# Optimization experiments

Hardware: AMD Instinct MI355X
Metric: run time of the kernel (lower is better)

## Reference

```python
import jax, jax.numpy as jnp
import numpy as np

B, S, D_IN, D_H = 16, 4096, 512, 512

def setup_inputs() -> dict:
    key = jax.random.key(0)
    ks = jax.random.split(key, 8)
    inp = {
        "input": jax.random.normal(ks[0], (B, D_IN), dtype=jnp.float32),
        "context": jax.random.normal(ks[1], (B, S, D_IN), dtype=jnp.float32),
        "mask": jax.random.bernoulli(ks[2], 0.2, (B, S)),
        # parameters (torch nn.Linear layout: W [out,in], b [out])
        "W_in": jax.random.normal(ks[3], (D_H, D_IN), dtype=jnp.float32) / np.sqrt(D_IN),
        "b_in": jax.random.normal(ks[4], (D_H,), dtype=jnp.float32) * 0.01,
        "W_ctx": jax.random.normal(ks[5], (D_H, D_IN), dtype=jnp.float32) / np.sqrt(D_IN),
        "b_ctx": jax.random.normal(ks[6], (D_H,), dtype=jnp.float32) * 0.01,
        "v": jax.random.normal(ks[7], (D_H,), dtype=jnp.float32),
    }
    return inp


def reference(input, context, mask, W_in, b_in, W_ctx, b_ctx, v):
    # inp: [B, H] projected decoder state
    inp = input @ W_in.T + b_in
    # ctx: [B, S, H] projected context (this is what the torch code matmuls
    # with the softmax weights, i.e. hidden lives in hidden_dim space)
    ctx = context @ W_ctx.T + b_ctx
    # additive (Bahdanau) scores: v . tanh(inp + ctx) -> [B, S]
    scores = jnp.einsum("h,bsh->bs", v, jnp.tanh(inp[:, None, :] + ctx))
    # masked positions get -inf so they receive zero softmax weight
    scores = jnp.where(mask, -jnp.inf, scores)
    attn = jax.nn.softmax(scores, axis=-1)  # [B, S]
    # weighted sum of projected context: [B, H]
    hidden = jnp.einsum("bsh,bs->bh", ctx, attn)
    return hidden, attn
```

## Files before the change

### kernel.cpp

```cpp
#include <hip/hip_runtime.h>
#include <hip/hip_bf16.h>

#define B_  16
#define S_  4096
#define DIN 512
#define DH  512

typedef _Float16 f16x8 __attribute__((ext_vector_type(8)));
typedef _Float16 f16x4 __attribute__((ext_vector_type(4)));
typedef float    f32x4 __attribute__((ext_vector_type(4)));


__device__ __forceinline__ float fast_tanh(float x) {
    float e = __expf(2.f * x);
    return 1.f - 2.f * __builtin_amdgcn_rcpf(e + 1.f);
}

__device__ __forceinline__ void gload_lds16(const void* g, void* l) {
    __builtin_amdgcn_global_load_lds(
        (const __attribute__((address_space(1))) void*)g,
        (__attribute__((address_space(3))) void*)l, 16, 0, 0);
}

__device__ __forceinline__ int mask_at(const void* mask, int isByte, int idx) {
    return isByte ? (int)((const unsigned char*)mask)[idx]
                  : ((const int*)mask)[idx];
}

__global__ void prep_kernel(const float* __restrict__ input,
                            const float* __restrict__ W_in,
                            const float* __restrict__ b_in,
                            const float* __restrict__ W_ctx,
                            const float* __restrict__ b_ctx,
                            const void*  __restrict__ mask,
                            _Float16* __restrict__ W16,
                            float* __restrict__ addv,
                            float* __restrict__ zeroRegion,
                            int* __restrict__ maskflag) {
    int blk = blockIdx.x;
    int tid = threadIdx.x;
    if (blk < 256) {
        int base = blk * 1024 + tid * 4;
        float4 wv = *(const float4*)(W_ctx + base);
        union { _Float16 f[4]; ushort4 u; } cv;
        cv.f[0] = (_Float16)wv.x; cv.f[1] = (_Float16)wv.y;
        cv.f[2] = (_Float16)wv.z; cv.f[3] = (_Float16)wv.w;
        *(ushort4*)(W16 + base) = cv.u;
    } else if (blk < 288) {
        int t = blk - 256;
        int b = t >> 1;
        int h = ((t & 1) << 8) + tid;
        __shared__ float inrow[DIN];
        inrow[tid]       = input[b * DIN + tid];
        inrow[tid + 256] = input[b * DIN + tid + 256];
        __syncthreads();
        const float* wr = W_in + (size_t)h * DIN;
        float acc = 0.f;
        for (int k = 0; k < DIN; k += 4) {
            float4 w4 = *(const float4*)(wr + k);
            acc += w4.x * inrow[k] + w4.y * inrow[k + 1]
                 + w4.z * inrow[k + 2] + w4.w * inrow[k + 3];
        }
        addv[b * DH + h] = acc + b_in[h] + b_ctx[h];
    } else if (blk == 288) {
        const uint4* m4 = (const uint4*)mask;
        unsigned int orw = 0;
#pragma unroll
        for (int it = 0; it < 16; ++it) {
            uint4 w = m4[it * 256 + tid];
            orw |= (w.x | w.y | w.z | w.w);
        }
        int found = ((orw & 0xFFFFFF00u) != 0) ? 1 : 0;
        __shared__ int f;
        if (tid == 0) f = 0;
        __syncthreads();
        if (found) atomicOr(&f, 1);
        __syncthreads();
        if (tid == 0) maskflag[0] = f;
    } else {
        int base = (blk - 289) * 4096;
#pragma unroll
        for (int it = 0; it < 16; ++it)
            zeroRegion[base + it * 256 + tid] = 0.f;
    }
}

__global__ __launch_bounds__(256)
void score_kernel(const float* __restrict__ context,
                  const _Float16* __restrict__ W16,
                  const float* __restrict__ addv,
                  const float* __restrict__ v,
                  float* __restrict__ scores) {
    __shared__ __align__(16) _Float16 As[2][4096];
    __shared__ __align__(16) _Float16 Bs[2][4096];

    const int tid  = threadIdx.x;
    const int wave = tid >> 6;
    const int lane = tid & 63;
    const int l15  = lane & 15;
    const int q    = lane >> 4;
    const int sg   = wave >> 1;
    const int ng   = wave & 1;

    const int xcd  = blockIdx.x & 7;
    const int slot = blockIdx.x >> 3;
    const int nt   = slot & 3;
    const int g    = (slot >> 2) * 8 + xcd;
    const int b    = g >> 5;
    const int st   = g & 31;
    const int s0   = st * 128;
    const int n0   = nt * 128;

    const float* ctxA = context + ((size_t)b * S_ + s0) * DIN;

#define STAGE_B(kc_, buf_)                                                     \
    {                                                                          \
        _Pragma("unroll")                                                      \
        for (int u = 0; u < 2; ++u) {                                          \
            int jn = wave * 2 + u;                                             \
            const _Float16* gp = W16 +                                         \
                (size_t)(n0 + jn * 16 + l15) * DIN + (kc_) * 32 + q * 8;       \
            gload_lds16(gp, &Bs[buf_][jn * 512]);                              \
        }                                                                      \
    }

    float4 areg[4];
#define LOADA(kc_)                                                             \
    {                                                                          \
        _Pragma("unroll")                                                      \
        for (int u = 0; u < 4; ++u) {                                          \
            int sgi = u * 256 + tid;                                           \
            int row = sgi >> 3, p = sgi & 7;                                   \
            areg[u] = *(const float4*)(ctxA + (size_t)row * DIN +              \
                                       (kc_) * 32 + p * 4);                    \
        }                                                                      \
    }

#define WRITEA(buf_)                                                           \
    {                                                                          \
        _Pragma("unroll")                                                      \
        for (int u = 0; u < 4; ++u) {                                          \
            int sgi = u * 256 + tid;                                           \
            int row = sgi >> 3, p = sgi & 7;                                   \
            int off = (row >> 4) * 512 + (p >> 1) * 128 + (row & 15) * 8 +     \
                      (p & 1) * 4;                                             \
            f16x4 hv;                                                          \
            hv[0] = (_Float16)areg[u].x; hv[1] = (_Float16)areg[u].y;          \
            hv[2] = (_Float16)areg[u].z; hv[3] = (_Float16)areg[u].w;          \
            *(f16x4*)&As[buf_][off] = hv;                                      \
        }                                                                      \
    }

    f32x4 acc[4][4];
#pragma unroll
    for (int jm = 0; jm < 4; ++jm)
#pragma unroll
        for (int jn = 0; jn < 4; ++jn) acc[jm][jn] = (f32x4){0.f, 0.f, 0.f, 0.f};

    STAGE_B(0, 0);
    LOADA(0);
    WRITEA(0);
    __syncthreads();

    for (int kc = 0; kc < 16; ++kc) {
        const int cur = kc & 1, nxt = cur ^ 1;
        if (kc + 1 < 16) {
            STAGE_B(kc + 1, nxt);
            LOADA(kc + 1);
        }

        f16x8 afr[4], bfr[4];
#pragma unroll
        for (int jm = 0; jm < 4; ++jm)
            afr[jm] = *(const f16x8*)&As[cur][(sg * 4 + jm) * 512 + q * 128 + l15 * 8];
#pragma unroll
        for (int jn = 0; jn < 4; ++jn)
            bfr[jn] = *(const f16x8*)&Bs[cur][(ng * 4 + jn) * 512 + q * 128 + l15 * 8];

#pragma unroll
        for (int jn = 0; jn < 4; ++jn)
#pragma unroll
            for (int jm = 0; jm < 4; ++jm)
                acc[jm][jn] = __builtin_amdgcn_mfma_f32_16x16x32_f16(
                    afr[jm], bfr[jn], acc[jm][jn], 0, 0, 0);

        if (kc + 1 < 16) WRITEA(nxt);
        __syncthreads();
    }

    const float* avb = addv + b * DH;
    float rowsum[4][4] = {{0.f,0.f,0.f,0.f},{0.f,0.f,0.f,0.f},
                          {0.f,0.f,0.f,0.f},{0.f,0.f,0.f,0.f}};
#pragma unroll
    for (int jn = 0; jn < 4; ++jn) {
        int n = n0 + (ng * 4 + jn) * 16 + l15;
        float av = avb[n];
        float vv = v[n];
#pragma unroll
        for (int jm = 0; jm < 4; ++jm)
#pragma unroll
            for (int r = 0; r < 4; ++r)
                rowsum[jm][r] += vv * fast_tanh(acc[jm][jn][r] + av);
    }
#pragma unroll
    for (int jm = 0; jm < 4; ++jm)
#pragma unroll
        for (int r = 0; r < 4; ++r) {
            float s = rowsum[jm][r];
            s += __shfl_xor(s, 1, 16);
            s += __shfl_xor(s, 2, 16);
            s += __shfl_xor(s, 4, 16);
            s += __shfl_xor(s, 8, 16);
            if (l15 == 0) {
                int srow = s0 + (sg * 4 + jm) * 16 + q * 4 + r;
                atomicAdd(&scores[b * S_ + srow], s);
            }
        }
}

__global__ __launch_bounds__(1024)
void stats_kernel(const float* __restrict__ scores,
                  const void* __restrict__ mask,
                  const int* __restrict__ maskflag,
                  float* __restrict__ stats) {
    __shared__ float rbuf[32];
    int b = blockIdx.x, tid = threadIdx.x;
    int wv = tid >> 6, ln = tid & 63;
    int isByte = maskflag[0];
    const float* sr = scores + b * S_;

    float mx = -__builtin_inff();
    float vals[4];
#pragma unroll
    for (int it = 0; it < 4; ++it) {
        int s = it * 1024 + tid;
        float x = mask_at(mask, isByte, b * S_ + s) ? -__builtin_inff() : sr[s];
        vals[it] = x;
        mx = fmaxf(mx, x);
    }
    for (int o = 1; o < 64; o <<= 1) mx = fmaxf(mx, __shfl_xor(mx, o, 64));
    if (ln == 0) rbuf[wv] = mx;
    __syncthreads();
    float m2 = rbuf[0];
#pragma unroll
    for (int i = 1; i < 16; ++i) m2 = fmaxf(m2, rbuf[i]);
    mx = m2;

    float sum = 0.f;
#pragma unroll
    for (int it = 0; it < 4; ++it) sum += __expf(vals[it] - mx);
    for (int o = 1; o < 64; o <<= 1) sum += __shfl_xor(sum, o, 64);
    if (ln == 0) rbuf[16 + wv] = sum;
    __syncthreads();
    if (tid == 0) {
        float t = 0.f;
#pragma unroll
        for (int i = 0; i < 16; ++i) t += rbuf[16 + i];
        stats[b * 2]     = mx;
        stats[b * 2 + 1] = 1.f / t;
    }
}

__global__ __launch_bounds__(256)
void attnwsum_kernel(const float* __restrict__ scores,
                     const float* __restrict__ context,
                     const void* __restrict__ mask,
                     const int* __restrict__ maskflag,
                     const float* __restrict__ stats,
                     float* __restrict__ attn,
                     float* __restrict__ wsum) {
    __shared__ int   selIdx[64];
    __shared__ float selW[64];
    __shared__ int   selCount;

    int b  = blockIdx.x >> 6;
    int c0 = (blockIdx.x & 63) * 64;
    int tid = threadIdx.x;
    int isByte = maskflag[0];
    float mx  = stats[b * 2];
    float inv = stats[b * 2 + 1];

    if (tid == 0) selCount = 0;
    __syncthreads();

    if (tid < 64) {
        int s = c0 + tid;
        int idx = b * S_ + s;
        float sc = mask_at(mask, isByte, idx) ? -__builtin_inff() : scores[idx];
        float p = __expf(sc - mx) * inv;
        attn[idx] = p;
        if (p > 1e-9f) {
            int k = atomicAdd(&selCount, 1);
            selIdx[k] = s;
            selW[k]  = p;
        }
    }
    __syncthreads();

    int cnt = selCount;
    if (cnt == 0) return;
    const float* cb = context + (size_t)b * S_ * DIN;
    float a00 = 0.f, a01 = 0.f, a10 = 0.f, a11 = 0.f;
    float a20 = 0.f, a21 = 0.f, a30 = 0.f, a31 = 0.f;
    int i = 0;
    for (; i + 4 <= cnt; i += 4) {
        const float* c0p = cb + (size_t)selIdx[i]     * DIN;
        const float* c1p = cb + (size_t)selIdx[i + 1] * DIN;
        const float* c2p = cb + (size_t)selIdx[i + 2] * DIN;
        const float* c3p = cb + (size_t)selIdx[i + 3] * DIN;
        float w0 = selW[i], w1 = selW[i + 1], w2 = selW[i + 2], w3 = selW[i + 3];
        a00 += w0 * c0p[tid]; a01 += w0 * c0p[tid + 256];
        a10 += w1 * c1p[tid]; a11 += w1 * c1p[tid + 256];
        a20 += w2 * c2p[tid]; a21 += w2 * c2p[tid + 256];
        a30 += w3 * c3p[tid]; a31 += w3 * c3p[tid + 256];
    }
    float acc0 = (a00 + a10) + (a20 + a30);
    float acc1 = (a01 + a11) + (a21 + a31);
    for (; i < cnt; ++i) {
        const float* cr = cb + (size_t)selIdx[i] * DIN;
        float w = selW[i];
        acc0 += w * cr[tid];
        acc1 += w * cr[tid + 256];
    }
    atomicAdd(&wsum[b * DIN + tid], acc0);
    atomicAdd(&wsum[b * DIN + tid + 256], acc1);
}

__global__ __launch_bounds__(256)
void hidden_kernel(const float* __restrict__ W_ctx,
                   const float* __restrict__ b_ctx,
                   const float* __restrict__ wsum,
                   float* __restrict__ hidden) {
    int b = blockIdx.x >> 1;
    int tid = threadIdx.x;
    int h = ((blockIdx.x & 1) << 8) + tid;
    __shared__ float wrow[DIN];
    wrow[tid]       = wsum[b * DIN + tid];
    wrow[tid + 256] = wsum[b * DIN + tid + 256];
    __syncthreads();
    const float* wr = W_ctx + (size_t)h * DIN;
    float acc = 0.f;
    for (int k = 0; k < DIN; k += 4) {
        float4 w4 = *(const float4*)(wr + k);
        acc += w4.x * wrow[k] + w4.y * wrow[k + 1]
             + w4.z * wrow[k + 2] + w4.w * wrow[k + 3];
    }
    hidden[b * DH + h] = acc + b_ctx[h];
}

extern "C" void kernel_launch(void* const* d_in, const int* in_sizes, int n_in,
                              void* d_out, int out_size, void* d_ws, size_t ws_size,
                              hipStream_t stream) {
    const float* input   = (const float*)d_in[0];
    const float* context = (const float*)d_in[1];
    const void*  mask    = d_in[2];
    const float* W_in    = (const float*)d_in[3];
    const float* b_in    = (const float*)d_in[4];
    const float* W_ctx   = (const float*)d_in[5];
    const float* b_ctx   = (const float*)d_in[6];
    const float* v       = (const float*)d_in[7];

    char* ws = (char*)d_ws;
    _Float16* W16   = (_Float16*)ws;
    float* addv     = (float*)(ws + 524288);
    float* scores   = (float*)(ws + 557056);
    float* wsum     = (float*)(ws + 819200);
    int*   maskflag = (int*)(ws + 851968);
    float* stats    = (float*)(ws + 852096);

    float* hidden = (float*)d_out;
    float* attn   = (float*)d_out + B_ * DH;

    prep_kernel<<<355, 256, 0, stream>>>(input, W_in, b_in, W_ctx, b_ctx, mask,
                                         W16, addv, scores , maskflag);
    score_kernel<<<2048, 256, 0, stream>>>(context, W16, addv, v, scores);
    stats_kernel<<<B_, 1024, 0, stream>>>(scores, mask, maskflag, stats);
    attnwsum_kernel<<<B_ * 64, 256, 0, stream>>>(scores, context, mask, maskflag,
                                                 stats, attn, wsum);
    hidden_kernel<<<B_ * 2, 256, 0, stream>>>(W_ctx, b_ctx, wsum, hidden);
}
```

Measured before the change: 312.7 us.

## Precast context to fp16 and stage it via direct LDS loads; fuse softmax stats

Adds a pass in the prep kernel that converts the whole context tensor to fp16 in workspace. The score GEMM then streams both operands with global-to-LDS loads instead of register loads plus conversion and LDS writes, which simplifies the loop to one barrier per step. The separate softmax-statistics kernel is removed, and each attention block recomputes its row's max and sum redundantly. The tradeoff is an extra full read and half-size write of the large context tensor, plus a larger workspace.

```diff
diff --git a/kernel.cpp b/kernel.cpp
--- a/kernel.cpp
+++ b/kernel.cpp
@@ -7,7 +7,6 @@
 #define DH  512
 
 typedef _Float16 f16x8 __attribute__((ext_vector_type(8)));
-typedef _Float16 f16x4 __attribute__((ext_vector_type(4)));
 typedef float    f32x4 __attribute__((ext_vector_type(4)));
 
 
@@ -27,27 +26,40 @@
                   : ((const int*)mask)[idx];
 }
 
-__global__ void prep_kernel(const float* __restrict__ input,
-                            const float* __restrict__ W_in,
-                            const float* __restrict__ b_in,
-                            const float* __restrict__ W_ctx,
-                            const float* __restrict__ b_ctx,
-                            const void*  __restrict__ mask,
-                            _Float16* __restrict__ W16,
-                            float* __restrict__ addv,
-                            float* __restrict__ zeroRegion,
-                            int* __restrict__ maskflag) {
+__global__ __launch_bounds__(256)
+void prep_kernel(const float* __restrict__ input,
+                 const float* __restrict__ W_in,
+                 const float* __restrict__ b_in,
+                 const float* __restrict__ context,
+                 const float* __restrict__ W_ctx,
+                 const float* __restrict__ b_ctx,
+                 const void*  __restrict__ mask,
+                 _Float16* __restrict__ W16,
+                 _Float16* __restrict__ ctx16,
+                 float* __restrict__ addv,
+                 float* __restrict__ zeroRegion,
+                 int* __restrict__ maskflag) {
     int blk = blockIdx.x;
     int tid = threadIdx.x;
-    if (blk < 256) {
-        int base = blk * 1024 + tid * 4;
+    if (blk < 8192) {
+#pragma unroll
+        for (int it = 0; it < 4; ++it) {
+            int base = blk * 4096 + it * 1024 + tid * 4;
+            float4 wv = *(const float4*)(context + base);
+            union { _Float16 f[4]; ushort4 u; } cv;
+            cv.f[0] = (_Float16)wv.x; cv.f[1] = (_Float16)wv.y;
+            cv.f[2] = (_Float16)wv.z; cv.f[3] = (_Float16)wv.w;
+            *(ushort4*)(ctx16 + base) = cv.u;
+        }
+    } else if (blk < 8448) {
+        int base = (blk - 8192) * 1024 + tid * 4;
         float4 wv = *(const float4*)(W_ctx + base);
         union { _Float16 f[4]; ushort4 u; } cv;
         cv.f[0] = (_Float16)wv.x; cv.f[1] = (_Float16)wv.y;
         cv.f[2] = (_Float16)wv.z; cv.f[3] = (_Float16)wv.w;
         *(ushort4*)(W16 + base) = cv.u;
-    } else if (blk < 288) {
-        int t = blk - 256;
+    } else if (blk < 8480) {
+        int t = blk - 8448;
         int b = t >> 1;
         int h = ((t & 1) << 8) + tid;
         __shared__ float inrow[DIN];
@@ -62,7 +74,7 @@
                  + w4.z * inrow[k + 2] + w4.w * inrow[k + 3];
         }
         addv[b * DH + h] = acc + b_in[h] + b_ctx[h];
-    } else if (blk == 288) {
+    } else if (blk == 8480) {
         const uint4* m4 = (const uint4*)mask;
         unsigned int orw = 0;
 #pragma unroll
@@ -78,7 +90,7 @@
         __syncthreads();
         if (tid == 0) maskflag[0] = f;
     } else {
-        int base = (blk - 289) * 4096;
+        int base = (blk - 8481) * 4096;
 #pragma unroll
         for (int it = 0; it < 16; ++it)
             zeroRegion[base + it * 256 + tid] = 0.f;
@@ -86,7 +98,7 @@
 }
 
 __global__ __launch_bounds__(256)
-void score_kernel(const float* __restrict__ context,
+void score_kernel(const _Float16* __restrict__ ctx16,
                   const _Float16* __restrict__ W16,
                   const float* __restrict__ addv,
                   const float* __restrict__ v,
@@ -111,71 +123,46 @@
     const int s0   = st * 128;
     const int n0   = nt * 128;
 
-    const float* ctxA = context + ((size_t)b * S_ + s0) * DIN;
-
-#define STAGE_B(kc_, buf_)                                                     \
-    {                                                                          \
-        _Pragma("unroll")                                                      \
-        for (int u = 0; u < 2; ++u) {                                          \
-            int jn = wave * 2 + u;                                             \
-            const _Float16* gp = W16 +                                         \
-                (size_t)(n0 + jn * 16 + l15) * DIN + (kc_) * 32 + q * 8;       \
-            gload_lds16(gp, &Bs[buf_][jn * 512]);                              \
-        }                                                                      \
-    }
-
-    float4 areg[4];
-#define LOADA(kc_)                                                             \
+    const _Float16* ctxA = ctx16 + ((size_t)b * S_ + s0) * DIN;
+
+#define STAGE(kc_, buf_)                                                       \
     {                                                                          \
         _Pragma("unroll")                                                      \
         for (int u = 0; u < 4; ++u) {                                          \
-            int sgi = u * 256 + tid;                                           \
-            int row = sgi >> 3, p = sgi & 7;                                   \
-            areg[u] = *(const float4*)(ctxA + (size_t)row * DIN +              \
-                                       (kc_) * 32 + p * 4);                    \
+            int id = wave * 4 + u;                                             \
+            if (id < 8) {                                                      \
+                const _Float16* gp = ctxA +                                    \
+                    (size_t)(id * 16 + l15) * DIN + (kc_) * 32 + q * 8;        \
+                gload_lds16(gp, &As[buf_][id * 512]);                          \
+            } else {                                                           \
+                int jn = id - 8;                                               \
+                const _Float16* gp = W16 +                                     \
+                    (size_t)(n0 + jn * 16 + l15) * DIN + (kc_) * 32 + q * 8;   \
+                gload_lds16(gp, &Bs[buf_][jn * 512]);                          \
+            }                                                                  \
         }                                                                      \
     }
 
-#define WRITEA(buf_)                                                           \
-    {                                                                          \
-        _Pragma("unroll")                                                      \
-        for (int u = 0; u < 4; ++u) {                                          \
-            int sgi = u * 256 + tid;                                           \
-            int row = sgi >> 3, p = sgi & 7;                                   \
-            int off = (row >> 4) * 512 + (p >> 1) * 128 + (row & 15) * 8 +     \
-                      (p & 1) * 4;                                             \
-            f16x4 hv;                                                          \
-            hv[0] = (_Float16)areg[u].x; hv[1] = (_Float16)areg[u].y;          \
-            hv[2] = (_Float16)areg[u].z; hv[3] = (_Float16)areg[u].w;          \
-            *(f16x4*)&As[buf_][off] = hv;                                      \
-        }                                                                      \
-    }
-
     f32x4 acc[4][4];
 #pragma unroll
     for (int jm = 0; jm < 4; ++jm)
 #pragma unroll
         for (int jn = 0; jn < 4; ++jn) acc[jm][jn] = (f32x4){0.f, 0.f, 0.f, 0.f};
 
-    STAGE_B(0, 0);
-    LOADA(0);
-    WRITEA(0);
-    __syncthreads();
+    STAGE(0, 0);
 
     for (int kc = 0; kc < 16; ++kc) {
-        const int cur = kc & 1, nxt = cur ^ 1;
-        if (kc + 1 < 16) {
-            STAGE_B(kc + 1, nxt);
-            LOADA(kc + 1);
-        }
+        __syncthreads();
+        int buf = kc & 1;
+        if (kc + 1 < 16) STAGE(kc + 1, buf ^ 1);
 
         f16x8 afr[4], bfr[4];
 #pragma unroll
         for (int jm = 0; jm < 4; ++jm)
-            afr[jm] = *(const f16x8*)&As[cur][(sg * 4 + jm) * 512 + q * 128 + l15 * 8];
+            afr[jm] = *(const f16x8*)&As[buf][(sg * 4 + jm) * 512 + q * 128 + l15 * 8];
 #pragma unroll
         for (int jn = 0; jn < 4; ++jn)
-            bfr[jn] = *(const f16x8*)&Bs[cur][(ng * 4 + jn) * 512 + q * 128 + l15 * 8];
+            bfr[jn] = *(const f16x8*)&Bs[buf][(ng * 4 + jn) * 512 + q * 128 + l15 * 8];
 
 #pragma unroll
         for (int jn = 0; jn < 4; ++jn)
@@ -183,9 +170,6 @@
             for (int jm = 0; jm < 4; ++jm)
                 acc[jm][jn] = __builtin_amdgcn_mfma_f32_16x16x32_f16(
                     afr[jm], bfr[jn], acc[jm][jn], 0, 0, 0);
-
-        if (kc + 1 < 16) WRITEA(nxt);
-        __syncthreads();
     }
 
     const float* avb = addv + b * DH;
@@ -218,57 +202,14 @@
         }
 }
 
-__global__ __launch_bounds__(1024)
-void stats_kernel(const float* __restrict__ scores,
-                  const void* __restrict__ mask,
-                  const int* __restrict__ maskflag,
-                  float* __restrict__ stats) {
-    __shared__ float rbuf[32];
-    int b = blockIdx.x, tid = threadIdx.x;
-    int wv = tid >> 6, ln = tid & 63;
-    int isByte = maskflag[0];
-    const float* sr = scores + b * S_;
-
-    float mx = -__builtin_inff();
-    float vals[4];
-#pragma unroll
-    for (int it = 0; it < 4; ++it) {
-        int s = it * 1024 + tid;
-        float x = mask_at(mask, isByte, b * S_ + s) ? -__builtin_inff() : sr[s];
-        vals[it] = x;
-        mx = fmaxf(mx, x);
-    }
-    for (int o = 1; o < 64; o <<= 1) mx = fmaxf(mx, __shfl_xor(mx, o, 64));
-    if (ln == 0) rbuf[wv] = mx;
-    __syncthreads();
-    float m2 = rbuf[0];
-#pragma unroll
-    for (int i = 1; i < 16; ++i) m2 = fmaxf(m2, rbuf[i]);
-    mx = m2;
-
-    float sum = 0.f;
-#pragma unroll
-    for (int it = 0; it < 4; ++it) sum += __expf(vals[it] - mx);
-    for (int o = 1; o < 64; o <<= 1) sum += __shfl_xor(sum, o, 64);
-    if (ln == 0) rbuf[16 + wv] = sum;
-    __syncthreads();
-    if (tid == 0) {
-        float t = 0.f;
-#pragma unroll
-        for (int i = 0; i < 16; ++i) t += rbuf[16 + i];
-        stats[b * 2]     = mx;
-        stats[b * 2 + 1] = 1.f / t;
-    }
-}
-
 __global__ __launch_bounds__(256)
 void attnwsum_kernel(const float* __restrict__ scores,
                      const float* __restrict__ context,
                      const void* __restrict__ mask,
                      const int* __restrict__ maskflag,
-                     const float* __restrict__ stats,
                      float* __restrict__ attn,
                      float* __restrict__ wsum) {
+    __shared__ float rbuf[8];
     __shared__ int   selIdx[64];
     __shared__ float selW[64];
     __shared__ int   selCount;
@@ -276,17 +217,37 @@
     int b  = blockIdx.x >> 6;
     int c0 = (blockIdx.x & 63) * 64;
     int tid = threadIdx.x;
+    int wv = tid >> 6, ln = tid & 63;
     int isByte = maskflag[0];
-    float mx  = stats[b * 2];
-    float inv = stats[b * 2 + 1];
-
+    const float* sr = scores + b * S_;
+
+    float mx = -__builtin_inff();
+    float vals[16];
+#pragma unroll
+    for (int it = 0; it < 16; ++it) {
+        int s = it * 256 + tid;
+        float x = mask_at(mask, isByte, b * S_ + s) ? -__builtin_inff() : sr[s];
+        vals[it] = x;
+        mx = fmaxf(mx, x);
+    }
+    for (int o = 1; o < 64; o <<= 1) mx = fmaxf(mx, __shfl_xor(mx, o, 64));
+    if (ln == 0) rbuf[wv] = mx;
+    __syncthreads();
+    mx = fmaxf(fmaxf(rbuf[0], rbuf[1]), fmaxf(rbuf[2], rbuf[3]));
+
+    float sum = 0.f;
+#pragma unroll
+    for (int it = 0; it < 16; ++it) sum += __expf(vals[it] - mx);
+    for (int o = 1; o < 64; o <<= 1) sum += __shfl_xor(sum, o, 64);
+    if (ln == 0) rbuf[4 + wv] = sum;
     if (tid == 0) selCount = 0;
     __syncthreads();
+    float inv = 1.f / (rbuf[4] + rbuf[5] + rbuf[6] + rbuf[7]);
 
     if (tid < 64) {
         int s = c0 + tid;
         int idx = b * S_ + s;
-        float sc = mask_at(mask, isByte, idx) ? -__builtin_inff() : scores[idx];
+        float sc = mask_at(mask, isByte, idx) ? -__builtin_inff() : sr[s];
         float p = __expf(sc - mx) * inv;
         attn[idx] = p;
         if (p > 1e-9f) {
@@ -362,20 +323,20 @@
 
     char* ws = (char*)d_ws;
     _Float16* W16   = (_Float16*)ws;
-    float* addv     = (float*)(ws + 524288);
-    float* scores   = (float*)(ws + 557056);
-    float* wsum     = (float*)(ws + 819200);
-    int*   maskflag = (int*)(ws + 851968);
-    float* stats    = (float*)(ws + 852096);
+    _Float16* ctx16 = (_Float16*)(ws + 524288);
+    float* addv     = (float*)(ws + 67633152);
+    float* scores   = (float*)(ws + 67665920);
+    float* wsum     = (float*)(ws + 67928064);
+    int*   maskflag = (int*)(ws + 67960832);
 
     float* hidden = (float*)d_out;
     float* attn   = (float*)d_out + B_ * DH;
 
-    prep_kernel<<<355, 256, 0, stream>>>(input, W_in, b_in, W_ctx, b_ctx, mask,
-                                         W16, addv, scores , maskflag);
-    score_kernel<<<2048, 256, 0, stream>>>(context, W16, addv, v, scores);
-    stats_kernel<<<B_, 1024, 0, stream>>>(scores, mask, maskflag, stats);
+    prep_kernel<<<8547, 256, 0, stream>>>(input, W_in, b_in, context, W_ctx,
+                                          b_ctx, mask, W16, ctx16, addv,
+                                          scores , maskflag);
+    score_kernel<<<2048, 256, 0, stream>>>(ctx16, W16, addv, v, scores);
     attnwsum_kernel<<<B_ * 64, 256, 0, stream>>>(scores, context, mask, maskflag,
-                                                 stats, attn, wsum);
+                                                 attn, wsum);
     hidden_kernel<<<B_ * 2, 256, 0, stream>>>(W_ctx, b_ctx, wsum, hidden);
 }
```

After: 323.0 us. 3.3% more time.
